# Kernel optimization log

Hardware: AMD Instinct MI355X
Metric: run time of the kernel (lower is better)

## Reference

```python
import jax, jax.numpy as jnp
import numpy as np

MARGIN = 1.0
BIG = 1e9  # stand-in for +inf to keep gradients NaN-free

def _l2_normalize(x, eps=1e-12):
    n = jnp.linalg.norm(x, axis=1, keepdims=True)
    return x / jnp.maximum(n, eps)

def setup_inputs() -> dict:
    key = jax.random.key(0)
    k1, k2, k3 = jax.random.split(key, 3)
    B, D = 4096, 1024
    return {
        "text_embeddings": jax.random.normal(k1, (B, D), dtype=jnp.float32),
        "graph_embeddings": jax.random.normal(k2, (B, D), dtype=jnp.float32),
        "labels": jax.random.randint(k3, (B,), 0, 512, dtype=jnp.int64),
    }

def reference(text_embeddings, graph_embeddings, labels):
    B = text_embeddings.shape[0]
    t = _l2_normalize(text_embeddings)
    g = _l2_normalize(graph_embeddings)
    # cosine distance matrix [B, B]
    distances = 1.0 - jnp.matmul(t, g.T)
    pos = jnp.diagonal(distances)                      # [B]
    neg_mask = labels[:, None] != labels[None, :]      # [B, B]
    has_neg = neg_mask.any(axis=1)                     # rows with >=1 negative
    # hard negative mining: per-row min over different-label columns
    hard_neg = jnp.min(jnp.where(neg_mask, distances, BIG), axis=1)
    per_row = jnp.where(has_neg, jax.nn.relu(pos - hard_neg + MARGIN), 0.0)
    triplet_loss = jnp.sum(per_row) / B
    return triplet_loss, distances
```

## Files before the change

kernel.cpp:

```cpp
#include <hip/hip_runtime.h>
#include <hip/hip_bf16.h>


typedef int i32x4 __attribute__((ext_vector_type(4)));

__device__ __forceinline__ void gload16(const void* g, void* l) {
  __builtin_amdgcn_global_load_lds(
      (__attribute__((address_space(1))) void*)(g),
      (__attribute__((address_space(3))) void*)(l), 16, 0, 0);
}

__device__ __forceinline__ int fkey(float x) {
  int u = __float_as_int(x);
  return u >= 0 ? u : (u ^ 0x7fffffff);
}
__device__ __forceinline__ float funkey(int k) {
  return __int_as_float(k >= 0 ? k : (k ^ 0x7fffffff));
}

__global__ __launch_bounds__(256) void k_quant(
    const float* __restrict__ t, const float* __restrict__ g,
    char4* __restrict__ qt, char4* __restrict__ qg,
    float* __restrict__ st, float* __restrict__ sg,
    int* __restrict__ hn_key, int D) {
  const int row = blockIdx.x;
  const float* src = (blockIdx.y ? g : t) + (size_t)row * D;
  char4*      dst  = (blockIdx.y ? qg : qt) + (size_t)row * (D >> 2);
  float*      sout = blockIdx.y ? sg : st;

  float4 v = ((const float4*)src)[threadIdx.x];
  float ss = v.x * v.x + v.y * v.y + v.z * v.z + v.w * v.w;
  float am = fmaxf(fmaxf(fabsf(v.x), fabsf(v.y)), fmaxf(fabsf(v.z), fabsf(v.w)));
#pragma unroll
  for (int off = 32; off; off >>= 1) {
    ss += __shfl_down(ss, off);
    am = fmaxf(am, __shfl_down(am, off));
  }
  __shared__ float rs[4], rm[4];
  if ((threadIdx.x & 63) == 0) { rs[threadIdx.x >> 6] = ss; rm[threadIdx.x >> 6] = am; }
  __syncthreads();
  const float ssT = rs[0] + rs[1] + rs[2] + rs[3];
  const float amT = fmaxf(fmaxf(rm[0], rm[1]), fmaxf(rm[2], rm[3]));
  const float qs  = 127.0f / fmaxf(amT, 1e-20f);

  char4 o;
  o.x = (char)__float2int_rn(v.x * qs);
  o.y = (char)__float2int_rn(v.y * qs);
  o.z = (char)__float2int_rn(v.z * qs);
  o.w = (char)__float2int_rn(v.w * qs);
  dst[threadIdx.x] = o;

  if (threadIdx.x == 0) {
    sout[row] = fmaxf(amT, 1e-20f) / (127.0f * fmaxf(sqrtf(ssT), 1e-12f));
    if (blockIdx.y == 0) hn_key[row] = __float_as_int(1e9f);
  }
}

__global__ __launch_bounds__(512, 2) void k_gemm_fused(
    const char* __restrict__ A, const char* __restrict__ Bm,
    const float* __restrict__ sA, const float* __restrict__ sB,
    const int* __restrict__ labels, float* __restrict__ Dout,
    int* __restrict__ hn_key, float* __restrict__ pos, int N, int K) {
  __shared__ __align__(16) char Abuf[2][256 * 128];
  __shared__ __align__(16) char Bbuf[2][256 * 128];
  __shared__ int   labR[256], labC[256], hnmin[256];
  __shared__ float sAr[256], sBc[256];

  const int tid  = threadIdx.x;
  const int lane = tid & 63;
  const int w    = tid >> 6;
  const int waveM = w >> 2, waveN = w & 3;

  const int nb  = N >> 8;
  const int cpx = (nb * nb) >> 3;
  const int bid = blockIdx.x;
  const int swz = (bid & 7) * cpx + (bid >> 3);
  const int rowBase = (swz / nb) * 256;
  const int colBase = (swz % nb) * 256;

  const int rr   = tid >> 3;
  const int scol = ((tid & 7) ^ (rr & 7)) << 4;
  const char* aS = A  + (size_t)(rowBase + rr) * K + scol;
  const char* bS = Bm + (size_t)(colBase + rr) * K + scol;
  const int ldsOff = tid * 16;

  const int sw  = (lane & 7) << 4;
  const int khi = (lane >> 4) << 4;
  const int kx0 = khi ^ sw;
  const int kx1 = (64 + khi) ^ sw;
  const int aBase = (waveM * 128 + (lane & 15)) * 128;
  const int bBase = (waveN * 64  + (lane & 15)) * 128;

  const int NT = K >> 7;

#pragma unroll
  for (int h = 0; h < 2; ++h)
#pragma unroll
    for (int j = 0; j < 2; ++j) {
      gload16(aS + (size_t)(h * 128 + j * 64) * K,
              &Abuf[0][h * 16384 + j * 8192 + ldsOff]);
      gload16(bS + (size_t)(h * 128 + j * 64) * K,
              &Bbuf[0][h * 16384 + j * 8192 + ldsOff]);
    }
  if (NT > 1) {
    gload16(aS + (size_t)128,                    &Abuf[1][0 * 8192 + ldsOff]);
    gload16(aS + (size_t)64 * K + 128,           &Abuf[1][1 * 8192 + ldsOff]);
  }
  if (tid < 256) {
    labR[tid]  = labels[rowBase + tid];
    sAr[tid]   = sA[rowBase + tid];
    hnmin[tid] = __float_as_int(1e9f);
  } else {
    labC[tid - 256] = labels[colBase + (tid - 256)];
    sBc[tid - 256]  = sB[colBase + (tid - 256)];
  }
  if (NT > 1) asm volatile("s_waitcnt vmcnt(2) lgkmcnt(0)" ::: "memory");
  else        asm volatile("s_waitcnt vmcnt(0) lgkmcnt(0)" ::: "memory");
  __builtin_amdgcn_s_barrier();
  asm volatile("" ::: "memory");

  i32x4 acc[8][4];
#pragma unroll
  for (int m = 0; m < 8; ++m)
#pragma unroll
    for (int n = 0; n < 4; ++n) acc[m][n] = (i32x4){0, 0, 0, 0};

  for (int t = 0; t < NT; ++t) {
    const int c = t & 1;
    const char* Ab = &Abuf[c][0];
    const char* Bb = &Bbuf[c][0];
    char* An = &Abuf[c ^ 1][0];
    char* Bn = &Bbuf[c ^ 1][0];
    const bool nx = (t + 1 < NT);
    const size_t ko1 = (size_t)(t + 1) * 128;

    i32x4 af[4][2], bf0[2][2], bf1[2][2];

#pragma unroll
    for (int m = 0; m < 4; ++m) {
      af[m][0] = *(const i32x4*)(Ab + aBase + m * 2048 + kx0);
      af[m][1] = *(const i32x4*)(Ab + aBase + m * 2048 + kx1);
    }
#pragma unroll
    for (int n = 0; n < 2; ++n) {
      bf0[n][0] = *(const i32x4*)(Bb + bBase + n * 2048 + kx0);
      bf0[n][1] = *(const i32x4*)(Bb + bBase + n * 2048 + kx1);
    }
    if (nx) {
      gload16(aS + (size_t)128 * K + ko1,        An + 16384 + ldsOff);
      gload16(aS + (size_t)192 * K + ko1,        An + 16384 + 8192 + ldsOff);
    }
    __builtin_amdgcn_s_barrier();
    __builtin_amdgcn_s_setprio(1);
#pragma unroll
    for (int ks = 0; ks < 2; ++ks)
#pragma unroll
      for (int m = 0; m < 4; ++m)
#pragma unroll
        for (int n = 0; n < 2; ++n)
          acc[m][n] = __builtin_amdgcn_mfma_i32_16x16x64_i8(
              af[m][ks], bf0[n][ks], acc[m][n], 0, 0, 0);
    __builtin_amdgcn_s_setprio(0);
    __builtin_amdgcn_s_barrier();

#pragma unroll
    for (int n = 0; n < 2; ++n) {
      bf1[n][0] = *(const i32x4*)(Bb + bBase + 4096 + n * 2048 + kx0);
      bf1[n][1] = *(const i32x4*)(Bb + bBase + 4096 + n * 2048 + kx1);
    }
    if (nx) {
      gload16(bS + ko1,                          Bn + ldsOff);
      gload16(bS + (size_t)64 * K + ko1,         Bn + 8192 + ldsOff);
    }
    __builtin_amdgcn_s_barrier();
    __builtin_amdgcn_s_setprio(1);
#pragma unroll
    for (int ks = 0; ks < 2; ++ks)
#pragma unroll
      for (int m = 0; m < 4; ++m)
#pragma unroll
        for (int n = 0; n < 2; ++n)
          acc[m][2 + n] = __builtin_amdgcn_mfma_i32_16x16x64_i8(
              af[m][ks], bf1[n][ks], acc[m][2 + n], 0, 0, 0);
    __builtin_amdgcn_s_setprio(0);
    __builtin_amdgcn_s_barrier();

#pragma unroll
    for (int m = 0; m < 4; ++m) {
      af[m][0] = *(const i32x4*)(Ab + aBase + 8192 + m * 2048 + kx0);
      af[m][1] = *(const i32x4*)(Ab + aBase + 8192 + m * 2048 + kx1);
    }
    if (nx) {
      gload16(bS + (size_t)128 * K + ko1,        Bn + 16384 + ldsOff);
      gload16(bS + (size_t)192 * K + ko1,        Bn + 16384 + 8192 + ldsOff);
    }
    __builtin_amdgcn_s_barrier();
    __builtin_amdgcn_s_setprio(1);
#pragma unroll
    for (int ks = 0; ks < 2; ++ks)
#pragma unroll
      for (int m = 0; m < 4; ++m)
#pragma unroll
        for (int n = 0; n < 2; ++n)
          acc[4 + m][2 + n] = __builtin_amdgcn_mfma_i32_16x16x64_i8(
              af[m][ks], bf1[n][ks], acc[4 + m][2 + n], 0, 0, 0);
    __builtin_amdgcn_s_setprio(0);
    __builtin_amdgcn_s_barrier();

    __builtin_amdgcn_s_setprio(1);
#pragma unroll
    for (int ks = 0; ks < 2; ++ks)
#pragma unroll
      for (int m = 0; m < 4; ++m)
#pragma unroll
        for (int n = 0; n < 2; ++n)
          acc[4 + m][n] = __builtin_amdgcn_mfma_i32_16x16x64_i8(
              af[m][ks], bf0[n][ks], acc[4 + m][n], 0, 0, 0);
    __builtin_amdgcn_s_setprio(0);
    __builtin_amdgcn_s_barrier();
    asm volatile("" ::: "memory");

    if (nx) {
      if (t + 2 < NT) {
        const size_t ko2 = (size_t)(t + 2) * 128;
        gload16(aS + ko2,                  &Abuf[c][0] + ldsOff);
        gload16(aS + (size_t)64 * K + ko2, &Abuf[c][0] + 8192 + ldsOff);
        asm volatile("s_waitcnt vmcnt(2)" ::: "memory");
      } else {
        asm volatile("s_waitcnt vmcnt(0)" ::: "memory");
      }
      __builtin_amdgcn_s_barrier();
      asm volatile("" ::: "memory");
    }
  }

  const int ci = lane & 15;
  const int r4 = (lane >> 4) << 2;
  const bool diagBlk = (rowBase == colBase);
#pragma unroll
  for (int m = 0; m < 8; ++m) {
    const int gilB = waveM * 128 + m * 16 + r4;
#pragma unroll
    for (int r = 0; r < 4; ++r) {
      const int gil = gilB + r;
      const int li  = labR[gil];
      const float sa = sAr[gil];
      const size_t gi = (size_t)(rowBase + gil);
      float mn = 1e9f;
#pragma unroll
      for (int n = 0; n < 4; ++n) {
        const int gjl = waveN * 64 + n * 16 + ci;
        const float d = 1.0f - sa * sBc[gjl] * (float)acc[m][n][r];
        Dout[gi * N + (colBase + gjl)] = d;
        if (labC[gjl] != li) mn = fminf(mn, d);
        if (diagBlk && gil == gjl) pos[gi] = d;
      }
#pragma unroll
      for (int off = 1; off < 16; off <<= 1) mn = fminf(mn, __shfl_xor(mn, off));
      if (ci == 0) atomicMin(&hnmin[gil], fkey(mn));
    }
  }
  __syncthreads();
  if (tid < 256) atomicMin(&hn_key[rowBase + tid], hnmin[tid]);
}

__global__ __launch_bounds__(256) void k_final(
    const int* __restrict__ hn_key, const float* __restrict__ pos,
    float* __restrict__ out, int N) {
  float s = 0.f;
  for (int i = threadIdx.x; i < N; i += 256) {
    const float hn = funkey(hn_key[i]);
    const float pr = pos[i] - hn + 1.0f;
    s += pr > 0.f ? pr : 0.f;
  }
#pragma unroll
  for (int off = 32; off; off >>= 1) s += __shfl_down(s, off);
  __shared__ float red[4];
  if ((threadIdx.x & 63) == 0) red[threadIdx.x >> 6] = s;
  __syncthreads();
  if (threadIdx.x == 0) out[0] = (red[0] + red[1] + red[2] + red[3]) / (float)N;
}

extern "C" void kernel_launch(void* const* d_in, const int* in_sizes, int n_in,
                              void* d_out, int out_size, void* d_ws, size_t ws_size,
                              hipStream_t stream) {
  const float* t      = (const float*)d_in[0];
  const float* g      = (const float*)d_in[1];
  const int*   labels = (const int*)d_in[2];
  const int Bn = in_sizes[2];
  const int D  = in_sizes[0] / Bn;

  float* out  = (float*)d_out;
  float* dist = out + 1;

  char*  qT     = (char*)d_ws;
  char*  qG     = qT + (size_t)Bn * D;
  float* sT     = (float*)(qG + (size_t)Bn * D);
  float* sG     = sT + Bn;
  int*   hn_key = (int*)(sG + Bn);
  float* pos    = (float*)(hn_key + Bn);

  k_quant<<<dim3(Bn, 2), 256, 0, stream>>>(t, g, (char4*)qT, (char4*)qG,
                                           sT, sG, hn_key, D);
  const int nb = Bn / 256;
  k_gemm_fused<<<dim3(nb * nb), 512, 0, stream>>>(qT, qG, sT, sG, labels, dist,
                                                  hn_key, pos, Bn, D);
  k_final<<<1, 256, 0, stream>>>(hn_key, pos, out, Bn);
}
```

Baseline: 49.90 us.

## Simplify GEMM prefetch to a plain double buffer with one barrier per tile

Result: no change. 50.58 us (+1.4%).

```diff
diff --git a/kernel.cpp b/kernel.cpp
--- a/kernel.cpp
+++ b/kernel.cpp
@@ -94,17 +94,9 @@
   const int NT = K >> 7;
 
 #pragma unroll
-  for (int h = 0; h < 2; ++h)
-#pragma unroll
-    for (int j = 0; j < 2; ++j) {
-      gload16(aS + (size_t)(h * 128 + j * 64) * K,
-              &Abuf[0][h * 16384 + j * 8192 + ldsOff]);
-      gload16(bS + (size_t)(h * 128 + j * 64) * K,
-              &Bbuf[0][h * 16384 + j * 8192 + ldsOff]);
-    }
-  if (NT > 1) {
-    gload16(aS + (size_t)128,                    &Abuf[1][0 * 8192 + ldsOff]);
-    gload16(aS + (size_t)64 * K + 128,           &Abuf[1][1 * 8192 + ldsOff]);
+  for (int j = 0; j < 4; ++j) {
+    gload16(aS + (size_t)(j * 64) * K, &Abuf[0][j * 8192 + ldsOff]);
+    gload16(bS + (size_t)(j * 64) * K, &Bbuf[0][j * 8192 + ldsOff]);
   }
   if (tid < 256) {
     labR[tid]  = labels[rowBase + tid];
@@ -114,8 +106,7 @@
     labC[tid - 256] = labels[colBase + (tid - 256)];
     sBc[tid - 256]  = sB[colBase + (tid - 256)];
   }
-  if (NT > 1) asm volatile("s_waitcnt vmcnt(2) lgkmcnt(0)" ::: "memory");
-  else        asm volatile("s_waitcnt vmcnt(0) lgkmcnt(0)" ::: "memory");
+  asm volatile("s_waitcnt vmcnt(0) lgkmcnt(0)" ::: "memory");
   __builtin_amdgcn_s_barrier();
   asm volatile("" ::: "memory");
 
@@ -134,6 +125,14 @@
     const bool nx = (t + 1 < NT);
     const size_t ko1 = (size_t)(t + 1) * 128;
 
+    if (nx) {
+#pragma unroll
+      for (int j = 0; j < 4; ++j) {
+        gload16(aS + (size_t)(j * 64) * K + ko1, An + j * 8192 + ldsOff);
+        gload16(bS + (size_t)(j * 64) * K + ko1, Bn + j * 8192 + ldsOff);
+      }
+    }
+
     i32x4 af[4][2], bf0[2][2], bf1[2][2];
 
 #pragma unroll
@@ -146,11 +145,6 @@
       bf0[n][0] = *(const i32x4*)(Bb + bBase + n * 2048 + kx0);
       bf0[n][1] = *(const i32x4*)(Bb + bBase + n * 2048 + kx1);
     }
-    if (nx) {
-      gload16(aS + (size_t)128 * K + ko1,        An + 16384 + ldsOff);
-      gload16(aS + (size_t)192 * K + ko1,        An + 16384 + 8192 + ldsOff);
-    }
-    __builtin_amdgcn_s_barrier();
     __builtin_amdgcn_s_setprio(1);
 #pragma unroll
     for (int ks = 0; ks < 2; ++ks)
@@ -161,18 +155,12 @@
           acc[m][n] = __builtin_amdgcn_mfma_i32_16x16x64_i8(
               af[m][ks], bf0[n][ks], acc[m][n], 0, 0, 0);
     __builtin_amdgcn_s_setprio(0);
-    __builtin_amdgcn_s_barrier();
 
 #pragma unroll
     for (int n = 0; n < 2; ++n) {
       bf1[n][0] = *(const i32x4*)(Bb + bBase + 4096 + n * 2048 + kx0);
       bf1[n][1] = *(const i32x4*)(Bb + bBase + 4096 + n * 2048 + kx1);
     }
-    if (nx) {
-      gload16(bS + ko1,                          Bn + ldsOff);
-      gload16(bS + (size_t)64 * K + ko1,         Bn + 8192 + ldsOff);
-    }
-    __builtin_amdgcn_s_barrier();
     __builtin_amdgcn_s_setprio(1);
 #pragma unroll
     for (int ks = 0; ks < 2; ++ks)
@@ -183,18 +171,12 @@
           acc[m][2 + n] = __builtin_amdgcn_mfma_i32_16x16x64_i8(
               af[m][ks], bf1[n][ks], acc[m][2 + n], 0, 0, 0);
     __builtin_amdgcn_s_setprio(0);
-    __builtin_amdgcn_s_barrier();
 
 #pragma unroll
     for (int m = 0; m < 4; ++m) {
       af[m][0] = *(const i32x4*)(Ab + aBase + 8192 + m * 2048 + kx0);
       af[m][1] = *(const i32x4*)(Ab + aBase + 8192 + m * 2048 + kx1);
     }
-    if (nx) {
-      gload16(bS + (size_t)128 * K + ko1,        Bn + 16384 + ldsOff);
-      gload16(bS + (size_t)192 * K + ko1,        Bn + 16384 + 8192 + ldsOff);
-    }
-    __builtin_amdgcn_s_barrier();
     __builtin_amdgcn_s_setprio(1);
 #pragma unroll
     for (int ks = 0; ks < 2; ++ks)
@@ -205,7 +187,6 @@
           acc[4 + m][2 + n] = __builtin_amdgcn_mfma_i32_16x16x64_i8(
               af[m][ks], bf1[n][ks], acc[4 + m][2 + n], 0, 0, 0);
     __builtin_amdgcn_s_setprio(0);
-    __builtin_amdgcn_s_barrier();
 
     __builtin_amdgcn_s_setprio(1);
 #pragma unroll
@@ -217,18 +198,9 @@
           acc[4 + m][n] = __builtin_amdgcn_mfma_i32_16x16x64_i8(
               af[m][ks], bf0[n][ks], acc[4 + m][n], 0, 0, 0);
     __builtin_amdgcn_s_setprio(0);
-    __builtin_amdgcn_s_barrier();
-    asm volatile("" ::: "memory");
 
     if (nx) {
-      if (t + 2 < NT) {
-        const size_t ko2 = (size_t)(t + 2) * 128;
-        gload16(aS + ko2,                  &Abuf[c][0] + ldsOff);
-        gload16(aS + (size_t)64 * K + ko2, &Abuf[c][0] + 8192 + ldsOff);
-        asm volatile("s_waitcnt vmcnt(2)" ::: "memory");
-      } else {
-        asm volatile("s_waitcnt vmcnt(0)" ::: "memory");
-      }
+      asm volatile("s_waitcnt vmcnt(0)" ::: "memory");
       __builtin_amdgcn_s_barrier();
       asm volatile("" ::: "memory");
     }
```
